# Performance work log

Hardware: AMD Instinct MI355X
Metric: run time of the kernel (lower is better)

## Reference

```python
import jax, jax.numpy as jnp
import numpy as np

N = 100000   # nodes
E = 1600000  # edges
I_DIM = 512
H_DIM = 64   # hardcoded in GCNEncoder
Z_DIM = 64


def gcn_conv(x, W, b, src, dst, n):
    """GCNConv: D^{-1/2}(A+I)D^{-1/2} X W + b, edge weights = 1."""
    xw = x @ W  # [n, out]
    ones = jnp.ones(src.shape[0], dtype=xw.dtype)
    deg = jax.ops.segment_sum(ones, dst, num_segments=n) + 1.0  # +1 for self-loop
    dinv = jax.lax.rsqrt(deg)
    norm = dinv[src] * dinv[dst]  # [E]
    agg = jax.ops.segment_sum(xw[src] * norm[:, None], dst, num_segments=n)
    agg = agg + xw * (dinv * dinv)[:, None]  # self-loop term, norm = 1/deg
    return agg + b


def setup_inputs() -> dict:
    key = jax.random.key(0)
    ks = jax.random.split(key, 9)
    x = jax.random.normal(ks[0], (N, I_DIM), dtype=jnp.float32)
    edge_index = jax.random.randint(ks[1], (2, E), 0, N, dtype=jnp.int64)
    # glorot-ish init for weights
    W1 = jax.random.normal(ks[2], (I_DIM, H_DIM), jnp.float32) * (1.0 / np.sqrt(I_DIM))
    b1 = jnp.zeros((H_DIM,), jnp.float32)
    W_mu = jax.random.normal(ks[3], (H_DIM, Z_DIM), jnp.float32) * (1.0 / np.sqrt(H_DIM))
    b_mu = jnp.zeros((Z_DIM,), jnp.float32)
    W_var = jax.random.normal(ks[4], (H_DIM, Z_DIM), jnp.float32) * (1.0 / np.sqrt(H_DIM))
    b_var = jnp.zeros((Z_DIM,), jnp.float32)
    eps = jax.random.normal(ks[5], (N, Z_DIM), jnp.float32)  # reparameterization noise
    return {"x": x, "edge_index": edge_index, "W1": W1, "b1": b1,
            "W_mu": W_mu, "b_mu": b_mu, "W_var": W_var, "b_var": b_var,
            "eps": eps}


def reference(x, edge_index, W1, b1, W_mu, b_mu, W_var, b_var, eps):
    n = x.shape[0]
    src, dst = edge_index[0], edge_index[1]
    # encoder (eval mode: dropout is identity)
    h = jax.nn.relu(gcn_conv(x, W1, b1, src, dst, n))
    z_mean = gcn_conv(h, W_mu, b_mu, src, dst, n)
    z_var = jax.nn.softplus(gcn_conv(h, W_var, b_var, src, dst, n))
    # Normal(z_mean, z_var).rsample()
    z = z_mean + z_var * eps
    return z_mean, z_var, z
```

## Files before the change

### kernel.cpp

```cpp
#include <hip/hip_runtime.h>
#include <hip/hip_bf16.h>
#include <math.h>

#define IDIM 512
#define HDIM 64

#define CB_SH 9
#define CB_NODES 512
#define PCHUNK 4096

typedef __attribute__((ext_vector_type(8))) short short8;
typedef __attribute__((ext_vector_type(4))) float f32x4;
typedef unsigned short u16;
typedef unsigned int u32;

__device__ __forceinline__ float bflo(u32 u) { return __uint_as_float(u << 16); }
__device__ __forceinline__ float bfhi(u32 u) { return __uint_as_float(u & 0xffff0000u); }


__global__ __launch_bounds__(256) void k_chist(const int* __restrict__ dst,
                                               int* __restrict__ gHist, int E, int NB) {
    __shared__ int h[1024];
    int tid = threadIdx.x;
    for (int i = tid; i < NB; i += 256) h[i] = 0;
    __syncthreads();
    int stride = gridDim.x * 256;
    for (int e = blockIdx.x * 256 + tid; e < E; e += stride)
        atomicAdd(&h[dst[e] >> CB_SH], 1);
    __syncthreads();
    for (int i = tid; i < NB; i += 256)
        if (h[i]) atomicAdd(&gHist[i], h[i]);
}

__global__ __launch_bounds__(256) void k_cscan(const int* __restrict__ gHist,
                                               int* __restrict__ bucketBase,
                                               int* __restrict__ gcur, int NB,
                                               int* __restrict__ rowptr, int n, int E) {
    __shared__ int ss[256];
    int tid = threadIdx.x;
    int v[4];
    int s = 0;
#pragma unroll
    for (int k = 0; k < 4; k++) {
        int i = tid * 4 + k;
        v[k] = (i < NB) ? gHist[i] : 0;
        s += v[k];
    }
    ss[tid] = s;
    __syncthreads();
    for (int o = 1; o < 256; o <<= 1) {
        int u = (tid >= o) ? ss[tid - o] : 0;
        __syncthreads();
        ss[tid] += u;
        __syncthreads();
    }
    int ex = ss[tid] - s;
#pragma unroll
    for (int k = 0; k < 4; k++) {
        int i = tid * 4 + k;
        if (i < NB) { bucketBase[i] = ex; gcur[i] = ex; }
        ex += v[k];
    }
    if (tid == 0) { bucketBase[NB] = E; rowptr[n] = E; }
}

__global__ __launch_bounds__(256) void k_partition(const int* __restrict__ src,
                                                   const int* __restrict__ dst,
                                                   int* __restrict__ gcur,
                                                   int2* __restrict__ tmp, int E, int NB) {
    __shared__ int h[1024];
    __shared__ int base[1024];
    int tid = threadIdx.x;
    int e0 = blockIdx.x * PCHUNK;
    int e1 = min(e0 + PCHUNK, E);
    for (int i = tid; i < NB; i += 256) h[i] = 0;
    __syncthreads();
    for (int e = e0 + tid; e < e1; e += 256)
        atomicAdd(&h[dst[e] >> CB_SH], 1);
    __syncthreads();
    for (int i = tid; i < NB; i += 256) {
        int c = h[i];
        base[i] = c ? atomicAdd(&gcur[i], c) : 0;
        h[i] = 0;
    }
    __syncthreads();
    for (int e = e0 + tid; e < e1; e += 256) {
        int d = dst[e];
        int b = d >> CB_SH;
        int r = atomicAdd(&h[b], 1);
        tmp[base[b] + r] = make_int2(src[e], d);
    }
}

__global__ __launch_bounds__(256) void k_finalize(const int2* __restrict__ tmp,
                                                  const int* __restrict__ bucketBase,
                                                  int* __restrict__ rowptr,
                                                  float* __restrict__ dinv,
                                                  int* __restrict__ srcs, int n) {
    __shared__ int hist[CB_NODES];
    __shared__ int off[CB_NODES];
    __shared__ int ss[256];
    int b = blockIdx.x;
    int tid = threadIdx.x;
    int node0 = b << CB_SH;
    int nloc = min(CB_NODES, n - node0);
    int e0 = bucketBase[b], e1 = bucketBase[b + 1];
    hist[tid] = 0;
    hist[tid + 256] = 0;
    __syncthreads();
    for (int e = e0 + tid; e < e1; e += 256)
        atomicAdd(&hist[tmp[e].y - node0], 1);
    __syncthreads();
    int v0 = hist[2 * tid], v1 = hist[2 * tid + 1];
    int ps = v0 + v1;
    ss[tid] = ps;
    __syncthreads();
    for (int o = 1; o < 256; o <<= 1) {
        int u = (tid >= o) ? ss[tid - o] : 0;
        __syncthreads();
        ss[tid] += u;
        __syncthreads();
    }
    int ex = ss[tid] - ps;
    off[2 * tid] = ex;
    off[2 * tid + 1] = ex + v0;
    __syncthreads();
    for (int i = tid; i < nloc; i += 256) {
        rowptr[node0 + i] = e0 + off[i];
        dinv[node0 + i] = rsqrtf((float)hist[i] + 1.0f);
    }
    __syncthreads();
    for (int e = e0 + tid; e < e1; e += 256) {
        int2 p = tmp[e];
        int r = atomicAdd(&off[p.y - node0], 1);
        srcs[e0 + r] = p.x;
    }
}

__global__ __launch_bounds__(256) void k_prepB(const float* __restrict__ W1,
                                               short* __restrict__ Btg) {
    int id = blockIdx.x * 256 + threadIdx.x;
    if (id >= IDIM * HDIM) return;
    int k = id >> 6, nn = id & 63;
    __hip_bfloat16 b = __float2bfloat16(W1[id]);
    Btg[nn * IDIM + k] = *(short*)&b;
}

__global__ __launch_bounds__(256) void k_prepW2(const float* __restrict__ Wmu,
                                                const float* __restrict__ Wvar,
                                                short* __restrict__ Whi,
                                                short* __restrict__ Wlo) {
    int id = blockIdx.x * 256 + threadIdx.x;
    if (id >= 128 * 64) return;
    int c = id >> 6;
    int k = id & 63;
    float wv = (c < 64) ? Wmu[k * 64 + c] : Wvar[k * 64 + (c - 64)];
    __hip_bfloat16 h = __float2bfloat16(wv);
    float hf = __bfloat162float(h);
    __hip_bfloat16 l = __float2bfloat16(wv - hf);
    Whi[c * 64 + k] = *(short*)&h;
    Wlo[c * 64 + k] = *(short*)&l;
}

#define GM 128
#define KC 64
#define APAD 8
__global__ __launch_bounds__(256) void k_gemm1(const float* __restrict__ x,
                                               const short* __restrict__ Btg,
                                               const float* __restrict__ dinv,
                                               u16* __restrict__ g1, int n) {
    __shared__ short As[GM][KC + APAD];
    __shared__ short Bs[HDIM][KC + APAD];
    int tid = threadIdx.x;
    int row0 = blockIdx.x * GM;
    int w = tid >> 6, lane = tid & 63;
    int m = lane & 15, kb = lane >> 4;

    f32x4 acc[2][4];
#pragma unroll
    for (int rb = 0; rb < 2; rb++)
#pragma unroll
        for (int nt = 0; nt < 4; nt++) acc[rb][nt] = (f32x4){0.f, 0.f, 0.f, 0.f};

    for (int kc = 0; kc < IDIM; kc += KC) {
        __syncthreads();
#pragma unroll
        for (int i = 0; i < 8; i++) {
            int idx = tid + i * 256;
            int r = idx >> 4;
            int c4 = idx & 15;
            int grow = row0 + r;
            float4 v = make_float4(0.f, 0.f, 0.f, 0.f);
            if (grow < n) v = *(const float4*)&x[(size_t)grow * IDIM + kc + c4 * 4];
            __hip_bfloat162 h0 = __float22bfloat162_rn(make_float2(v.x, v.y));
            __hip_bfloat162 h1 = __float22bfloat162_rn(make_float2(v.z, v.w));
            int2 p;
            p.x = *(int*)&h0;
            p.y = *(int*)&h1;
            *(int2*)&As[r][c4 * 4] = p;
        }
#pragma unroll
        for (int i = 0; i < 2; i++) {
            int idx = tid + i * 256;
            int r = idx >> 3;
            int u8 = idx & 7;
            float4 v = *(const float4*)&Btg[(size_t)r * IDIM + kc + u8 * 8];
            *(float4*)&Bs[r][u8 * 8] = v;
        }
        __syncthreads();
#pragma unroll
        for (int ks = 0; ks < KC; ks += 32) {
            short8 a0 = *(const short8*)&As[w * 32 + m][ks + kb * 8];
            short8 a1 = *(const short8*)&As[w * 32 + 16 + m][ks + kb * 8];
            short8 b0 = *(const short8*)&Bs[m][ks + kb * 8];
            short8 b1 = *(const short8*)&Bs[16 + m][ks + kb * 8];
            short8 b2 = *(const short8*)&Bs[32 + m][ks + kb * 8];
            short8 b3 = *(const short8*)&Bs[48 + m][ks + kb * 8];
            acc[0][0] = __builtin_amdgcn_mfma_f32_16x16x32_bf16(a0, b0, acc[0][0], 0, 0, 0);
            acc[0][1] = __builtin_amdgcn_mfma_f32_16x16x32_bf16(a0, b1, acc[0][1], 0, 0, 0);
            acc[0][2] = __builtin_amdgcn_mfma_f32_16x16x32_bf16(a0, b2, acc[0][2], 0, 0, 0);
            acc[0][3] = __builtin_amdgcn_mfma_f32_16x16x32_bf16(a0, b3, acc[0][3], 0, 0, 0);
            acc[1][0] = __builtin_amdgcn_mfma_f32_16x16x32_bf16(a1, b0, acc[1][0], 0, 0, 0);
            acc[1][1] = __builtin_amdgcn_mfma_f32_16x16x32_bf16(a1, b1, acc[1][1], 0, 0, 0);
            acc[1][2] = __builtin_amdgcn_mfma_f32_16x16x32_bf16(a1, b2, acc[1][2], 0, 0, 0);
            acc[1][3] = __builtin_amdgcn_mfma_f32_16x16x32_bf16(a1, b3, acc[1][3], 0, 0, 0);
        }
    }
#pragma unroll
    for (int rb = 0; rb < 2; rb++) {
        int rbase = row0 + w * 32 + rb * 16 + kb * 4;
#pragma unroll
        for (int reg = 0; reg < 4; reg++) {
            int grow = rbase + reg;
            if (grow < n) {
                float dv = dinv[grow];
#pragma unroll
                for (int nt = 0; nt < 4; nt++) {
                    __hip_bfloat16 b = __float2bfloat16(acc[rb][nt][reg] * dv);
                    g1[(size_t)grow * HDIM + nt * 16 + m] = *(u16*)&b;
                }
            }
        }
    }
}

__global__ __launch_bounds__(256) void k_gather1(const int* __restrict__ rowptr,
                                                 const int* __restrict__ srcs,
                                                 const float* __restrict__ dinv,
                                                 const u16* __restrict__ g1,
                                                 const float* __restrict__ b1,
                                                 u16* __restrict__ g2, int n) {
    int tid = threadIdx.x;
    int r = tid >> 6, lane = tid & 63;
    int grp = lane >> 3, q = lane & 7;
    int i = blockIdx.x * 4 + r;
    if (i >= n) return;
    int beg = rowptr[i], end = rowptr[i + 1];
    float a[8];
#pragma unroll
    for (int k = 0; k < 8; k++) a[k] = 0.f;
    int j = beg + grp;
    for (; j + 8 < end; j += 16) {
        int s0 = srcs[j];
        int s1 = srcs[j + 8];
        uint4 u0 = *(const uint4*)&g1[(size_t)s0 * HDIM + q * 8];
        uint4 u1 = *(const uint4*)&g1[(size_t)s1 * HDIM + q * 8];
        a[0] += bflo(u0.x) + bflo(u1.x); a[1] += bfhi(u0.x) + bfhi(u1.x);
        a[2] += bflo(u0.y) + bflo(u1.y); a[3] += bfhi(u0.y) + bfhi(u1.y);
        a[4] += bflo(u0.z) + bflo(u1.z); a[5] += bfhi(u0.z) + bfhi(u1.z);
        a[6] += bflo(u0.w) + bflo(u1.w); a[7] += bfhi(u0.w) + bfhi(u1.w);
    }
    if (j < end) {
        int s0 = srcs[j];
        uint4 u0 = *(const uint4*)&g1[(size_t)s0 * HDIM + q * 8];
        a[0] += bflo(u0.x); a[1] += bfhi(u0.x);
        a[2] += bflo(u0.y); a[3] += bfhi(u0.y);
        a[4] += bflo(u0.z); a[5] += bfhi(u0.z);
        a[6] += bflo(u0.w); a[7] += bfhi(u0.w);
    }
#pragma unroll
    for (int k = 0; k < 8; k++) {
        a[k] += __shfl_xor(a[k], 8);
        a[k] += __shfl_xor(a[k], 16);
        a[k] += __shfl_xor(a[k], 32);
    }
    if (grp == 0) {
        uint4 us = *(const uint4*)&g1[(size_t)i * HDIM + q * 8];
        float s0 = bflo(us.x), s1 = bfhi(us.x), s2 = bflo(us.y), s3 = bfhi(us.y);
        float s4 = bflo(us.z), s5 = bfhi(us.z), s6 = bflo(us.w), s7 = bfhi(us.w);
        float4 bv0 = *(const float4*)&b1[q * 8];
        float4 bv1 = *(const float4*)&b1[q * 8 + 4];
        float di = dinv[i];
        float o0 = fmaxf(di * (a[0] + s0) + bv0.x, 0.f) * di;
        float o1 = fmaxf(di * (a[1] + s1) + bv0.y, 0.f) * di;
        float o2 = fmaxf(di * (a[2] + s2) + bv0.z, 0.f) * di;
        float o3 = fmaxf(di * (a[3] + s3) + bv0.w, 0.f) * di;
        float o4 = fmaxf(di * (a[4] + s4) + bv1.x, 0.f) * di;
        float o5 = fmaxf(di * (a[5] + s5) + bv1.y, 0.f) * di;
        float o6 = fmaxf(di * (a[6] + s6) + bv1.z, 0.f) * di;
        float o7 = fmaxf(di * (a[7] + s7) + bv1.w, 0.f) * di;
        __hip_bfloat162 p0 = __float22bfloat162_rn(make_float2(o0, o1));
        __hip_bfloat162 p1 = __float22bfloat162_rn(make_float2(o2, o3));
        __hip_bfloat162 p2 = __float22bfloat162_rn(make_float2(o4, o5));
        __hip_bfloat162 p3 = __float22bfloat162_rn(make_float2(o6, o7));
        uint4 w;
        w.x = *(u32*)&p0; w.y = *(u32*)&p1; w.z = *(u32*)&p2; w.w = *(u32*)&p3;
        *(uint4*)&g2[(size_t)i * HDIM + q * 8] = w;
    }
}

__global__ __launch_bounds__(256) void k_gather2(const int* __restrict__ rowptr,
                                                 const int* __restrict__ srcs,
                                                 const float* __restrict__ dinv,
                                                 const u16* __restrict__ g2,
                                                 float* __restrict__ hagg, int n) {
    int tid = threadIdx.x;
    int r = tid >> 6, lane = tid & 63;
    int grp = lane >> 3, q = lane & 7;
    int i = blockIdx.x * 4 + r;
    if (i >= n) return;
    int beg = rowptr[i], end = rowptr[i + 1];
    float a[8];
#pragma unroll
    for (int k = 0; k < 8; k++) a[k] = 0.f;
    int j = beg + grp;
    for (; j + 8 < end; j += 16) {
        int s0 = srcs[j];
        int s1 = srcs[j + 8];
        uint4 u0 = *(const uint4*)&g2[(size_t)s0 * HDIM + q * 8];
        uint4 u1 = *(const uint4*)&g2[(size_t)s1 * HDIM + q * 8];
        a[0] += bflo(u0.x) + bflo(u1.x); a[1] += bfhi(u0.x) + bfhi(u1.x);
        a[2] += bflo(u0.y) + bflo(u1.y); a[3] += bfhi(u0.y) + bfhi(u1.y);
        a[4] += bflo(u0.z) + bflo(u1.z); a[5] += bfhi(u0.z) + bfhi(u1.z);
        a[6] += bflo(u0.w) + bflo(u1.w); a[7] += bfhi(u0.w) + bfhi(u1.w);
    }
    if (j < end) {
        int s0 = srcs[j];
        uint4 u0 = *(const uint4*)&g2[(size_t)s0 * HDIM + q * 8];
        a[0] += bflo(u0.x); a[1] += bfhi(u0.x);
        a[2] += bflo(u0.y); a[3] += bfhi(u0.y);
        a[4] += bflo(u0.z); a[5] += bfhi(u0.z);
        a[6] += bflo(u0.w); a[7] += bfhi(u0.w);
    }
#pragma unroll
    for (int k = 0; k < 8; k++) {
        a[k] += __shfl_xor(a[k], 8);
        a[k] += __shfl_xor(a[k], 16);
        a[k] += __shfl_xor(a[k], 32);
    }
    if (grp == 0) {
        uint4 us = *(const uint4*)&g2[(size_t)i * HDIM + q * 8];
        float di = dinv[i];
        float4 o0, o1;
        o0.x = di * (a[0] + bflo(us.x));
        o0.y = di * (a[1] + bfhi(us.x));
        o0.z = di * (a[2] + bflo(us.y));
        o0.w = di * (a[3] + bfhi(us.y));
        o1.x = di * (a[4] + bflo(us.z));
        o1.y = di * (a[5] + bfhi(us.z));
        o1.z = di * (a[6] + bflo(us.w));
        o1.w = di * (a[7] + bfhi(us.w));
        *(float4*)&hagg[(size_t)i * HDIM + q * 8] = o0;
        *(float4*)&hagg[(size_t)i * HDIM + q * 8 + 4] = o1;
    }
}

__global__ __launch_bounds__(256) void k_gemm2(const float* __restrict__ hagg,
                                               const short* __restrict__ Whi,
                                               const short* __restrict__ Wlo,
                                               const float* __restrict__ bmu,
                                               const float* __restrict__ bvar,
                                               const float* __restrict__ eps,
                                               float* __restrict__ out, int n) {
    int tid = threadIdx.x;
    int w = tid >> 6, lane = tid & 63;
    int m = lane & 15, kb = lane >> 4;
    int row0 = blockIdx.x * 128 + w * 32;

    short8 ah[2][2], al[2][2];
#pragma unroll
    for (int rb = 0; rb < 2; rb++) {
#pragma unroll
        for (int ks = 0; ks < 2; ks++) {
            int grow = row0 + rb * 16 + m;
            float v[8];
            if (grow < n) {
                const float* base = &hagg[(size_t)grow * HDIM + ks * 32 + kb * 8];
                float4 v0 = *(const float4*)base;
                float4 v1 = *(const float4*)(base + 4);
                v[0] = v0.x; v[1] = v0.y; v[2] = v0.z; v[3] = v0.w;
                v[4] = v1.x; v[5] = v1.y; v[6] = v1.z; v[7] = v1.w;
            } else {
#pragma unroll
                for (int jj = 0; jj < 8; jj++) v[jj] = 0.f;
            }
#pragma unroll
            for (int jj = 0; jj < 8; jj++) {
                __hip_bfloat16 h = __float2bfloat16(v[jj]);
                float hf = __bfloat162float(h);
                __hip_bfloat16 l = __float2bfloat16(v[jj] - hf);
                ah[rb][ks][jj] = *(short*)&h;
                al[rb][ks][jj] = *(short*)&l;
            }
        }
    }

    f32x4 acc[2][8];
#pragma unroll
    for (int rb = 0; rb < 2; rb++)
#pragma unroll
        for (int nt = 0; nt < 8; nt++) acc[rb][nt] = (f32x4){0.f, 0.f, 0.f, 0.f};

#pragma unroll
    for (int nt = 0; nt < 8; nt++) {
#pragma unroll
        for (int ks = 0; ks < 2; ks++) {
            const short* bbase = &Whi[(size_t)(nt * 16 + m) * HDIM + ks * 32 + kb * 8];
            const short* lbase = &Wlo[(size_t)(nt * 16 + m) * HDIM + ks * 32 + kb * 8];
            short8 bh = *(const short8*)bbase;
            short8 bl = *(const short8*)lbase;
#pragma unroll
            for (int rb = 0; rb < 2; rb++) {
                acc[rb][nt] = __builtin_amdgcn_mfma_f32_16x16x32_bf16(ah[rb][ks], bh, acc[rb][nt], 0, 0, 0);
                acc[rb][nt] = __builtin_amdgcn_mfma_f32_16x16x32_bf16(al[rb][ks], bh, acc[rb][nt], 0, 0, 0);
                acc[rb][nt] = __builtin_amdgcn_mfma_f32_16x16x32_bf16(ah[rb][ks], bl, acc[rb][nt], 0, 0, 0);
            }
        }
    }

    size_t nh = (size_t)n * HDIM;
#pragma unroll
    for (int rb = 0; rb < 2; rb++) {
#pragma unroll
        for (int nt = 0; nt < 4; nt++) {
            int c = nt * 16 + m;
            float bm = bmu[c], bv = bvar[c];
#pragma unroll
            for (int reg = 0; reg < 4; reg++) {
                int grow = row0 + rb * 16 + kb * 4 + reg;
                if (grow < n) {
                    float mu = acc[rb][nt][reg] + bm;
                    float va = acc[rb][nt + 4][reg] + bv;
                    float zv = fmaxf(va, 0.f) + log1pf(expf(-fabsf(va)));
                    size_t o = (size_t)grow * HDIM + c;
                    float z = mu + zv * eps[o];
                    out[o] = mu;
                    out[nh + o] = zv;
                    out[2 * nh + o] = z;
                }
            }
        }
    }
}

extern "C" void kernel_launch(void* const* d_in, const int* in_sizes, int n_in,
                              void* d_out, int out_size, void* d_ws, size_t ws_size,
                              hipStream_t stream) {
    const float* x    = (const float*)d_in[0];
    const int*   ei   = (const int*)d_in[1];
    const float* W1   = (const float*)d_in[2];
    const float* b1   = (const float*)d_in[3];
    const float* Wmu  = (const float*)d_in[4];
    const float* bmu  = (const float*)d_in[5];
    const float* Wvar = (const float*)d_in[6];
    const float* bvar = (const float*)d_in[7];
    const float* eps  = (const float*)d_in[8];
    float* out = (float*)d_out;

    int n = in_sizes[0] / IDIM;
    int E = in_sizes[1] / 2;
    const int* src = ei;
    const int* dst = ei + E;

    int NB = (n + CB_NODES - 1) >> CB_SH;

    char* p = (char*)d_ws;
    u16* bufB   = (u16*)p;               p += (size_t)n * HDIM * 2;
    float* hagg = (float*)p;             p += (size_t)n * HDIM * 4;
    u16* bufA   = (u16*)hagg;
    int2* tmp   = (int2*)hagg;
    int* srcs   = (int*)p;               p += (size_t)E * 4;
    short* Btg  = (short*)p;             p += (size_t)IDIM * HDIM * 2;
    short* W2hi = (short*)p;             p += (size_t)128 * HDIM * 2;
    short* W2lo = (short*)p;             p += (size_t)128 * HDIM * 2;
    int* rowptr = (int*)p;               p += (size_t)(n + 1) * 4;
    float* dinv = (float*)p;             p += (size_t)n * 4;
    int* gHist  = (int*)p;               p += 1024 * 4;
    int* gcur   = (int*)p;               p += 1024 * 4;
    int* bucketBase = (int*)p;           p += 1025 * 4;

    hipMemsetAsync(gHist, 0, (size_t)NB * sizeof(int), stream);
    k_chist<<<512, 256, 0, stream>>>(dst, gHist, E, NB);
    k_cscan<<<1, 256, 0, stream>>>(gHist, bucketBase, gcur, NB, rowptr, n, E);
    k_partition<<<(E + PCHUNK - 1) / PCHUNK, 256, 0, stream>>>(src, dst, gcur, tmp, E, NB);
    k_finalize<<<NB, 256, 0, stream>>>(tmp, bucketBase, rowptr, dinv, srcs, n);

    k_prepB<<<(IDIM * HDIM + 255) / 256, 256, 0, stream>>>(W1, Btg);
    k_prepW2<<<(128 * HDIM + 255) / 256, 256, 0, stream>>>(Wmu, Wvar, W2hi, W2lo);

    k_gemm1<<<(n + GM - 1) / GM, 256, 0, stream>>>(x, Btg, dinv, bufA, n);
    k_gather1<<<(n + 3) / 4, 256, 0, stream>>>(rowptr, srcs, dinv, bufA, b1, bufB, n);

    k_gather2<<<(n + 3) / 4, 256, 0, stream>>>(rowptr, srcs, dinv, bufB, hagg, n);
    k_gemm2<<<(n + 127) / 128, 256, 0, stream>>>(hagg, W2hi, W2lo, bmu, bvar, eps, out, n);
}
```

Baseline: 574.0 us.

## Split gather feature tables into 16-column slabs processed in separate grid passes

The first GEMM now writes its bf16 output as four column-major slabs of 16 features per node instead of 64-feature rows. Both gather kernels launch a 2D grid with one y-slice per slab, so each pass reads a 32-byte slab per neighbour. The goal is a smaller per-pass working set (about 3.2MB instead of 12.8MB) that fits better in L2 for random neighbour access. In exchange, rowptr and srcs are read four times, loads shrink to 4 bytes per lane, and many more blocks are launched.

```diff
diff --git a/kernel.cpp b/kernel.cpp
--- a/kernel.cpp
+++ b/kernel.cpp
@@ -237,7 +237,7 @@
 #pragma unroll
                 for (int nt = 0; nt < 4; nt++) {
                     __hip_bfloat16 b = __float2bfloat16(acc[rb][nt][reg] * dv);
-                    g1[(size_t)grow * HDIM + nt * 16 + m] = *(u16*)&b;
+                    g1[((size_t)nt * n + grow) * 16 + m] = *(u16*)&b;
                 }
             }
         }
@@ -247,121 +247,83 @@
 __global__ __launch_bounds__(256) void k_gather1(const int* __restrict__ rowptr,
                                                  const int* __restrict__ srcs,
                                                  const float* __restrict__ dinv,
-                                                 const u16* __restrict__ g1,
+                                                 const u16* __restrict__ g1s,
                                                  const float* __restrict__ b1,
-                                                 u16* __restrict__ g2, int n) {
+                                                 u16* __restrict__ g2s, int n) {
+    int pass = blockIdx.y;
+    const u16* T = g1s + (size_t)pass * n * 16;
+    u16* O = g2s + (size_t)pass * n * 16;
     int tid = threadIdx.x;
     int r = tid >> 6, lane = tid & 63;
     int grp = lane >> 3, q = lane & 7;
     int i = blockIdx.x * 4 + r;
     if (i >= n) return;
     int beg = rowptr[i], end = rowptr[i + 1];
-    float a[8];
-#pragma unroll
-    for (int k = 0; k < 8; k++) a[k] = 0.f;
+    float a0 = 0.f, a1 = 0.f;
     int j = beg + grp;
     for (; j + 8 < end; j += 16) {
         int s0 = srcs[j];
         int s1 = srcs[j + 8];
-        uint4 u0 = *(const uint4*)&g1[(size_t)s0 * HDIM + q * 8];
-        uint4 u1 = *(const uint4*)&g1[(size_t)s1 * HDIM + q * 8];
-        a[0] += bflo(u0.x) + bflo(u1.x); a[1] += bfhi(u0.x) + bfhi(u1.x);
-        a[2] += bflo(u0.y) + bflo(u1.y); a[3] += bfhi(u0.y) + bfhi(u1.y);
-        a[4] += bflo(u0.z) + bflo(u1.z); a[5] += bfhi(u0.z) + bfhi(u1.z);
-        a[6] += bflo(u0.w) + bflo(u1.w); a[7] += bfhi(u0.w) + bfhi(u1.w);
+        u32 u0 = *(const u32*)&T[(size_t)s0 * 16 + q * 2];
+        u32 u1 = *(const u32*)&T[(size_t)s1 * 16 + q * 2];
+        a0 += bflo(u0) + bflo(u1);
+        a1 += bfhi(u0) + bfhi(u1);
     }
     if (j < end) {
-        int s0 = srcs[j];
-        uint4 u0 = *(const uint4*)&g1[(size_t)s0 * HDIM + q * 8];
-        a[0] += bflo(u0.x); a[1] += bfhi(u0.x);
-        a[2] += bflo(u0.y); a[3] += bfhi(u0.y);
-        a[4] += bflo(u0.z); a[5] += bfhi(u0.z);
-        a[6] += bflo(u0.w); a[7] += bfhi(u0.w);
-    }
-#pragma unroll
-    for (int k = 0; k < 8; k++) {
-        a[k] += __shfl_xor(a[k], 8);
-        a[k] += __shfl_xor(a[k], 16);
-        a[k] += __shfl_xor(a[k], 32);
-    }
+        u32 u0 = *(const u32*)&T[(size_t)srcs[j] * 16 + q * 2];
+        a0 += bflo(u0);
+        a1 += bfhi(u0);
+    }
+    a0 += __shfl_xor(a0, 8); a0 += __shfl_xor(a0, 16); a0 += __shfl_xor(a0, 32);
+    a1 += __shfl_xor(a1, 8); a1 += __shfl_xor(a1, 16); a1 += __shfl_xor(a1, 32);
     if (grp == 0) {
-        uint4 us = *(const uint4*)&g1[(size_t)i * HDIM + q * 8];
-        float s0 = bflo(us.x), s1 = bfhi(us.x), s2 = bflo(us.y), s3 = bfhi(us.y);
-        float s4 = bflo(us.z), s5 = bfhi(us.z), s6 = bflo(us.w), s7 = bfhi(us.w);
-        float4 bv0 = *(const float4*)&b1[q * 8];
-        float4 bv1 = *(const float4*)&b1[q * 8 + 4];
+        u32 us = *(const u32*)&T[(size_t)i * 16 + q * 2];
+        float2 bv = *(const float2*)&b1[pass * 16 + q * 2];
         float di = dinv[i];
-        float o0 = fmaxf(di * (a[0] + s0) + bv0.x, 0.f) * di;
-        float o1 = fmaxf(di * (a[1] + s1) + bv0.y, 0.f) * di;
-        float o2 = fmaxf(di * (a[2] + s2) + bv0.z, 0.f) * di;
-        float o3 = fmaxf(di * (a[3] + s3) + bv0.w, 0.f) * di;
-        float o4 = fmaxf(di * (a[4] + s4) + bv1.x, 0.f) * di;
-        float o5 = fmaxf(di * (a[5] + s5) + bv1.y, 0.f) * di;
-        float o6 = fmaxf(di * (a[6] + s6) + bv1.z, 0.f) * di;
-        float o7 = fmaxf(di * (a[7] + s7) + bv1.w, 0.f) * di;
-        __hip_bfloat162 p0 = __float22bfloat162_rn(make_float2(o0, o1));
-        __hip_bfloat162 p1 = __float22bfloat162_rn(make_float2(o2, o3));
-        __hip_bfloat162 p2 = __float22bfloat162_rn(make_float2(o4, o5));
-        __hip_bfloat162 p3 = __float22bfloat162_rn(make_float2(o6, o7));
-        uint4 w;
-        w.x = *(u32*)&p0; w.y = *(u32*)&p1; w.z = *(u32*)&p2; w.w = *(u32*)&p3;
-        *(uint4*)&g2[(size_t)i * HDIM + q * 8] = w;
+        float o0 = fmaxf(di * (a0 + bflo(us)) + bv.x, 0.f) * di;
+        float o1 = fmaxf(di * (a1 + bfhi(us)) + bv.y, 0.f) * di;
+        __hip_bfloat162 pk = __float22bfloat162_rn(make_float2(o0, o1));
+        *(u32*)&O[(size_t)i * 16 + q * 2] = *(u32*)&pk;
     }
 }
 
 __global__ __launch_bounds__(256) void k_gather2(const int* __restrict__ rowptr,
                                                  const int* __restrict__ srcs,
                                                  const float* __restrict__ dinv,
-                                                 const u16* __restrict__ g2,
+                                                 const u16* __restrict__ g2s,
                                                  float* __restrict__ hagg, int n) {
+    int pass = blockIdx.y;
+    const u16* T = g2s + (size_t)pass * n * 16;
     int tid = threadIdx.x;
     int r = tid >> 6, lane = tid & 63;
     int grp = lane >> 3, q = lane & 7;
     int i = blockIdx.x * 4 + r;
     if (i >= n) return;
     int beg = rowptr[i], end = rowptr[i + 1];
-    float a[8];
-#pragma unroll
-    for (int k = 0; k < 8; k++) a[k] = 0.f;
+    float a0 = 0.f, a1 = 0.f;
     int j = beg + grp;
     for (; j + 8 < end; j += 16) {
         int s0 = srcs[j];
         int s1 = srcs[j + 8];
-        uint4 u0 = *(const uint4*)&g2[(size_t)s0 * HDIM + q * 8];
-        uint4 u1 = *(const uint4*)&g2[(size_t)s1 * HDIM + q * 8];
-        a[0] += bflo(u0.x) + bflo(u1.x); a[1] += bfhi(u0.x) + bfhi(u1.x);
-        a[2] += bflo(u0.y) + bflo(u1.y); a[3] += bfhi(u0.y) + bfhi(u1.y);
-        a[4] += bflo(u0.z) + bflo(u1.z); a[5] += bfhi(u0.z) + bfhi(u1.z);
-        a[6] += bflo(u0.w) + bflo(u1.w); a[7] += bfhi(u0.w) + bfhi(u1.w);
+        u32 u0 = *(const u32*)&T[(size_t)s0 * 16 + q * 2];
+        u32 u1 = *(const u32*)&T[(size_t)s1 * 16 + q * 2];
+        a0 += bflo(u0) + bflo(u1);
+        a1 += bfhi(u0) + bfhi(u1);
     }
     if (j < end) {
-        int s0 = srcs[j];
-        uint4 u0 = *(const uint4*)&g2[(size_t)s0 * HDIM + q * 8];
-        a[0] += bflo(u0.x); a[1] += bfhi(u0.x);
-        a[2] += bflo(u0.y); a[3] += bfhi(u0.y);
-        a[4] += bflo(u0.z); a[5] += bfhi(u0.z);
-        a[6] += bflo(u0.w); a[7] += bfhi(u0.w);
-    }
-#pragma unroll
-    for (int k = 0; k < 8; k++) {
-        a[k] += __shfl_xor(a[k], 8);
-        a[k] += __shfl_xor(a[k], 16);
-        a[k] += __shfl_xor(a[k], 32);
-    }
+        u32 u0 = *(const u32*)&T[(size_t)srcs[j] * 16 + q * 2];
+        a0 += bflo(u0);
+        a1 += bfhi(u0);
+    }
+    a0 += __shfl_xor(a0, 8); a0 += __shfl_xor(a0, 16); a0 += __shfl_xor(a0, 32);
+    a1 += __shfl_xor(a1, 8); a1 += __shfl_xor(a1, 16); a1 += __shfl_xor(a1, 32);
     if (grp == 0) {
-        uint4 us = *(const uint4*)&g2[(size_t)i * HDIM + q * 8];
+        u32 us = *(const u32*)&T[(size_t)i * 16 + q * 2];
         float di = dinv[i];
-        float4 o0, o1;
-        o0.x = di * (a[0] + bflo(us.x));
-        o0.y = di * (a[1] + bfhi(us.x));
-        o0.z = di * (a[2] + bflo(us.y));
-        o0.w = di * (a[3] + bfhi(us.y));
-        o1.x = di * (a[4] + bflo(us.z));
-        o1.y = di * (a[5] + bfhi(us.z));
-        o1.z = di * (a[6] + bflo(us.w));
-        o1.w = di * (a[7] + bfhi(us.w));
-        *(float4*)&hagg[(size_t)i * HDIM + q * 8] = o0;
-        *(float4*)&hagg[(size_t)i * HDIM + q * 8 + 4] = o1;
+        float2 o;
+        o.x = di * (a0 + bflo(us));
+        o.y = di * (a1 + bfhi(us));
+        *(float2*)&hagg[(size_t)i * HDIM + pass * 16 + q * 2] = o;
     }
 }
 
@@ -499,8 +461,9 @@
     k_prepW2<<<(128 * HDIM + 255) / 256, 256, 0, stream>>>(Wmu, Wvar, W2hi, W2lo);
 
     k_gemm1<<<(n + GM - 1) / GM, 256, 0, stream>>>(x, Btg, dinv, bufA, n);
-    k_gather1<<<(n + 3) / 4, 256, 0, stream>>>(rowptr, srcs, dinv, bufA, b1, bufB, n);
-
-    k_gather2<<<(n + 3) / 4, 256, 0, stream>>>(rowptr, srcs, dinv, bufB, hagg, n);
+    dim3 gg((n + 3) / 4, 4);
+    k_gather1<<<gg, 256, 0, stream>>>(rowptr, srcs, dinv, bufA, b1, bufB, n);
+
+    k_gather2<<<gg, 256, 0, stream>>>(rowptr, srcs, dinv, bufB, hagg, n);
     k_gemm2<<<(n + 127) / 128, 256, 0, stream>>>(hagg, W2hi, W2lo, bmu, bvar, eps, out, n);
 }
```

After: 721.2 us. 25.6% more time.

## Split gathers into source-range passes for cache locality with partial accumulation

Applied to the files above, without the earlier changes.

Edges are bucketed by source quarter as well as destination block, giving four CSR row-pointer sets. Each gather then runs as four passes, and each pass reads only a quarter of the feature table so that slice can stay in L2/MALL. Partial sums go through an fp32 scratch buffer using nontemporal loads and stores, and srcs reads are made nontemporal. The cost is more kernel launches, extra read-modify-write traffic on the accumulator, and a separate dinv kernel.

```diff
diff --git a/kernel.cpp b/kernel.cpp
--- a/kernel.cpp
+++ b/kernel.cpp
@@ -6,36 +6,42 @@
 #define HDIM 64
 
 #define CB_SH 9
-#define CB_NODES 512
+#define NSB 4
 #define PCHUNK 4096
 
 typedef __attribute__((ext_vector_type(8))) short short8;
 typedef __attribute__((ext_vector_type(4))) float f32x4;
+typedef __attribute__((ext_vector_type(4))) float f4;
 typedef unsigned short u16;
 typedef unsigned int u32;
 
 __device__ __forceinline__ float bflo(u32 u) { return __uint_as_float(u << 16); }
 __device__ __forceinline__ float bfhi(u32 u) { return __uint_as_float(u & 0xffff0000u); }
-
-
-__global__ __launch_bounds__(256) void k_chist(const int* __restrict__ dst,
-                                               int* __restrict__ gHist, int E, int NB) {
+__device__ __forceinline__ f4 ntload4(const float* p) { return __builtin_nontemporal_load((const f4*)p); }
+__device__ __forceinline__ void ntstore4(float* p, f4 v) { __builtin_nontemporal_store(v, (f4*)p); }
+
+__global__ __launch_bounds__(256) void k_chist(const int* __restrict__ src,
+                                               const int* __restrict__ dst,
+                                               int* __restrict__ gHist, int E,
+                                               int NBK, int NBd, int Q) {
     __shared__ int h[1024];
     int tid = threadIdx.x;
-    for (int i = tid; i < NB; i += 256) h[i] = 0;
+    for (int i = tid; i < NBK; i += 256) h[i] = 0;
     __syncthreads();
     int stride = gridDim.x * 256;
-    for (int e = blockIdx.x * 256 + tid; e < E; e += stride)
-        atomicAdd(&h[dst[e] >> CB_SH], 1);
-    __syncthreads();
-    for (int i = tid; i < NB; i += 256)
+    for (int e = blockIdx.x * 256 + tid; e < E; e += stride) {
+        int key = (src[e] / Q) * NBd + (dst[e] >> CB_SH);
+        atomicAdd(&h[key], 1);
+    }
+    __syncthreads();
+    for (int i = tid; i < NBK; i += 256)
         if (h[i]) atomicAdd(&gHist[i], h[i]);
 }
 
 __global__ __launch_bounds__(256) void k_cscan(const int* __restrict__ gHist,
                                                int* __restrict__ bucketBase,
-                                               int* __restrict__ gcur, int NB,
-                                               int* __restrict__ rowptr, int n, int E) {
+                                               int* __restrict__ gcur, int NBK, int NBd,
+                                               int* __restrict__ rowptr4, int n, int E) {
     __shared__ int ss[256];
     int tid = threadIdx.x;
     int v[4];
@@ -43,7 +49,7 @@
 #pragma unroll
     for (int k = 0; k < 4; k++) {
         int i = tid * 4 + k;
-        v[k] = (i < NB) ? gHist[i] : 0;
+        v[k] = (i < NBK) ? gHist[i] : 0;
         s += v[k];
     }
     ss[tid] = s;
@@ -58,53 +64,64 @@
 #pragma unroll
     for (int k = 0; k < 4; k++) {
         int i = tid * 4 + k;
-        if (i < NB) { bucketBase[i] = ex; gcur[i] = ex; }
+        if (i < NBK) {
+            bucketBase[i] = ex;
+            gcur[i] = ex;
+            if (i > 0 && (i % NBd) == 0)
+                rowptr4[(size_t)(i / NBd - 1) * (n + 1) + n] = ex;
+        }
         ex += v[k];
     }
-    if (tid == 0) { bucketBase[NB] = E; rowptr[n] = E; }
+    if (tid == 0) {
+        bucketBase[NBK] = E;
+        rowptr4[(size_t)(NSB - 1) * (n + 1) + n] = E;
+    }
 }
 
 __global__ __launch_bounds__(256) void k_partition(const int* __restrict__ src,
                                                    const int* __restrict__ dst,
                                                    int* __restrict__ gcur,
-                                                   int2* __restrict__ tmp, int E, int NB) {
+                                                   int2* __restrict__ tmp, int E,
+                                                   int NBK, int NBd, int Q) {
     __shared__ int h[1024];
     __shared__ int base[1024];
     int tid = threadIdx.x;
     int e0 = blockIdx.x * PCHUNK;
     int e1 = min(e0 + PCHUNK, E);
-    for (int i = tid; i < NB; i += 256) h[i] = 0;
-    __syncthreads();
-    for (int e = e0 + tid; e < e1; e += 256)
-        atomicAdd(&h[dst[e] >> CB_SH], 1);
-    __syncthreads();
-    for (int i = tid; i < NB; i += 256) {
+    for (int i = tid; i < NBK; i += 256) h[i] = 0;
+    __syncthreads();
+    for (int e = e0 + tid; e < e1; e += 256) {
+        int key = (src[e] / Q) * NBd + (dst[e] >> CB_SH);
+        atomicAdd(&h[key], 1);
+    }
+    __syncthreads();
+    for (int i = tid; i < NBK; i += 256) {
         int c = h[i];
         base[i] = c ? atomicAdd(&gcur[i], c) : 0;
         h[i] = 0;
     }
     __syncthreads();
     for (int e = e0 + tid; e < e1; e += 256) {
-        int d = dst[e];
-        int b = d >> CB_SH;
-        int r = atomicAdd(&h[b], 1);
-        tmp[base[b] + r] = make_int2(src[e], d);
+        int sv = src[e], d = dst[e];
+        int key = (sv / Q) * NBd + (d >> CB_SH);
+        int r = atomicAdd(&h[key], 1);
+        tmp[base[key] + r] = make_int2(sv, d);
     }
 }
 
 __global__ __launch_bounds__(256) void k_finalize(const int2* __restrict__ tmp,
                                                   const int* __restrict__ bucketBase,
-                                                  int* __restrict__ rowptr,
-                                                  float* __restrict__ dinv,
-                                                  int* __restrict__ srcs, int n) {
-    __shared__ int hist[CB_NODES];
-    __shared__ int off[CB_NODES];
+                                                  int* __restrict__ rowptr4,
+                                                  int* __restrict__ srcs, int n, int NBd) {
+    __shared__ int hist[1 << CB_SH];
+    __shared__ int off[1 << CB_SH];
     __shared__ int ss[256];
-    int b = blockIdx.x;
-    int tid = threadIdx.x;
-    int node0 = b << CB_SH;
-    int nloc = min(CB_NODES, n - node0);
-    int e0 = bucketBase[b], e1 = bucketBase[b + 1];
+    int key = blockIdx.x;
+    int sb = key / NBd, db = key % NBd;
+    int tid = threadIdx.x;
+    int node0 = db << CB_SH;
+    int nloc = min(1 << CB_SH, n - node0);
+    int e0 = bucketBase[key], e1 = bucketBase[key + 1];
     hist[tid] = 0;
     hist[tid + 256] = 0;
     __syncthreads();
@@ -125,16 +142,28 @@
     off[2 * tid] = ex;
     off[2 * tid + 1] = ex + v0;
     __syncthreads();
-    for (int i = tid; i < nloc; i += 256) {
-        rowptr[node0 + i] = e0 + off[i];
-        dinv[node0 + i] = rsqrtf((float)hist[i] + 1.0f);
-    }
+    int* rp = rowptr4 + (size_t)sb * (n + 1);
+    for (int i = tid; i < nloc; i += 256)
+        rp[node0 + i] = e0 + off[i];
     __syncthreads();
     for (int e = e0 + tid; e < e1; e += 256) {
         int2 p = tmp[e];
         int r = atomicAdd(&off[p.y - node0], 1);
         srcs[e0 + r] = p.x;
     }
+}
+
+__global__ __launch_bounds__(256) void k_dinv(const int* __restrict__ rowptr4,
+                                              float* __restrict__ dinv, int n) {
+    int i = blockIdx.x * 256 + threadIdx.x;
+    if (i >= n) return;
+    int d = 0;
+#pragma unroll
+    for (int sb = 0; sb < NSB; sb++) {
+        const int* rp = rowptr4 + (size_t)sb * (n + 1);
+        d += rp[i + 1] - rp[i];
+    }
+    dinv[i] = rsqrtf((float)d + 1.0f);
 }
 
 __global__ __launch_bounds__(256) void k_prepB(const float* __restrict__ W1,
@@ -244,25 +273,28 @@
     }
 }
 
-__global__ __launch_bounds__(256) void k_gather1(const int* __restrict__ rowptr,
-                                                 const int* __restrict__ srcs,
-                                                 const float* __restrict__ dinv,
-                                                 const u16* __restrict__ g1,
-                                                 const float* __restrict__ b1,
-                                                 u16* __restrict__ g2, int n) {
+__global__ __launch_bounds__(256) void k_g1pass(const int* __restrict__ rowptr4,
+                                                const int* __restrict__ srcs,
+                                                const float* __restrict__ dinv,
+                                                const u16* __restrict__ g1,
+                                                const float* __restrict__ b1,
+                                                float* __restrict__ acc1,
+                                                u16* __restrict__ g2, int n,
+                                                int pass, int isFirst, int isLast) {
+    const int* rp = rowptr4 + (size_t)pass * (n + 1);
     int tid = threadIdx.x;
     int r = tid >> 6, lane = tid & 63;
     int grp = lane >> 3, q = lane & 7;
     int i = blockIdx.x * 4 + r;
     if (i >= n) return;
-    int beg = rowptr[i], end = rowptr[i + 1];
+    int beg = rp[i], end = rp[i + 1];
     float a[8];
 #pragma unroll
     for (int k = 0; k < 8; k++) a[k] = 0.f;
     int j = beg + grp;
     for (; j + 8 < end; j += 16) {
-        int s0 = srcs[j];
-        int s1 = srcs[j + 8];
+        int s0 = __builtin_nontemporal_load(&srcs[j]);
+        int s1 = __builtin_nontemporal_load(&srcs[j + 8]);
         uint4 u0 = *(const uint4*)&g1[(size_t)s0 * HDIM + q * 8];
         uint4 u1 = *(const uint4*)&g1[(size_t)s1 * HDIM + q * 8];
         a[0] += bflo(u0.x) + bflo(u1.x); a[1] += bfhi(u0.x) + bfhi(u1.x);
@@ -271,7 +303,7 @@
         a[6] += bflo(u0.w) + bflo(u1.w); a[7] += bfhi(u0.w) + bfhi(u1.w);
     }
     if (j < end) {
-        int s0 = srcs[j];
+        int s0 = __builtin_nontemporal_load(&srcs[j]);
         uint4 u0 = *(const uint4*)&g1[(size_t)s0 * HDIM + q * 8];
         a[0] += bflo(u0.x); a[1] += bfhi(u0.x);
         a[2] += bflo(u0.y); a[3] += bfhi(u0.y);
@@ -285,48 +317,64 @@
         a[k] += __shfl_xor(a[k], 32);
     }
     if (grp == 0) {
-        uint4 us = *(const uint4*)&g1[(size_t)i * HDIM + q * 8];
-        float s0 = bflo(us.x), s1 = bfhi(us.x), s2 = bflo(us.y), s3 = bfhi(us.y);
-        float s4 = bflo(us.z), s5 = bfhi(us.z), s6 = bflo(us.w), s7 = bfhi(us.w);
-        float4 bv0 = *(const float4*)&b1[q * 8];
-        float4 bv1 = *(const float4*)&b1[q * 8 + 4];
-        float di = dinv[i];
-        float o0 = fmaxf(di * (a[0] + s0) + bv0.x, 0.f) * di;
-        float o1 = fmaxf(di * (a[1] + s1) + bv0.y, 0.f) * di;
-        float o2 = fmaxf(di * (a[2] + s2) + bv0.z, 0.f) * di;
-        float o3 = fmaxf(di * (a[3] + s3) + bv0.w, 0.f) * di;
-        float o4 = fmaxf(di * (a[4] + s4) + bv1.x, 0.f) * di;
-        float o5 = fmaxf(di * (a[5] + s5) + bv1.y, 0.f) * di;
-        float o6 = fmaxf(di * (a[6] + s6) + bv1.z, 0.f) * di;
-        float o7 = fmaxf(di * (a[7] + s7) + bv1.w, 0.f) * di;
-        __hip_bfloat162 p0 = __float22bfloat162_rn(make_float2(o0, o1));
-        __hip_bfloat162 p1 = __float22bfloat162_rn(make_float2(o2, o3));
-        __hip_bfloat162 p2 = __float22bfloat162_rn(make_float2(o4, o5));
-        __hip_bfloat162 p3 = __float22bfloat162_rn(make_float2(o6, o7));
-        uint4 w;
-        w.x = *(u32*)&p0; w.y = *(u32*)&p1; w.z = *(u32*)&p2; w.w = *(u32*)&p3;
-        *(uint4*)&g2[(size_t)i * HDIM + q * 8] = w;
-    }
-}
-
-__global__ __launch_bounds__(256) void k_gather2(const int* __restrict__ rowptr,
-                                                 const int* __restrict__ srcs,
-                                                 const float* __restrict__ dinv,
-                                                 const u16* __restrict__ g2,
-                                                 float* __restrict__ hagg, int n) {
+        size_t base = (size_t)i * HDIM + q * 8;
+        if (!isFirst) {
+            f4 p0 = ntload4(&acc1[base]);
+            f4 p1 = ntload4(&acc1[base + 4]);
+            a[0] += p0[0]; a[1] += p0[1]; a[2] += p0[2]; a[3] += p0[3];
+            a[4] += p1[0]; a[5] += p1[1]; a[6] += p1[2]; a[7] += p1[3];
+        }
+        if (!isLast) {
+            f4 s0v = {a[0], a[1], a[2], a[3]};
+            f4 s1v = {a[4], a[5], a[6], a[7]};
+            ntstore4(&acc1[base], s0v);
+            ntstore4(&acc1[base + 4], s1v);
+        } else {
+            uint4 us = *(const uint4*)&g1[base];
+            float s0 = bflo(us.x), s1 = bfhi(us.x), s2 = bflo(us.y), s3 = bfhi(us.y);
+            float s4 = bflo(us.z), s5 = bfhi(us.z), s6 = bflo(us.w), s7 = bfhi(us.w);
+            float4 bv0 = *(const float4*)&b1[q * 8];
+            float4 bv1 = *(const float4*)&b1[q * 8 + 4];
+            float di = dinv[i];
+            float o0 = fmaxf(di * (a[0] + s0) + bv0.x, 0.f) * di;
+            float o1 = fmaxf(di * (a[1] + s1) + bv0.y, 0.f) * di;
+            float o2 = fmaxf(di * (a[2] + s2) + bv0.z, 0.f) * di;
+            float o3 = fmaxf(di * (a[3] + s3) + bv0.w, 0.f) * di;
+            float o4 = fmaxf(di * (a[4] + s4) + bv1.x, 0.f) * di;
+            float o5 = fmaxf(di * (a[5] + s5) + bv1.y, 0.f) * di;
+            float o6 = fmaxf(di * (a[6] + s6) + bv1.z, 0.f) * di;
+            float o7 = fmaxf(di * (a[7] + s7) + bv1.w, 0.f) * di;
+            __hip_bfloat162 p0 = __float22bfloat162_rn(make_float2(o0, o1));
+            __hip_bfloat162 p1 = __float22bfloat162_rn(make_float2(o2, o3));
+            __hip_bfloat162 p2 = __float22bfloat162_rn(make_float2(o4, o5));
+            __hip_bfloat162 p3 = __float22bfloat162_rn(make_float2(o6, o7));
+            uint4 w;
+            w.x = *(u32*)&p0; w.y = *(u32*)&p1; w.z = *(u32*)&p2; w.w = *(u32*)&p3;
+            *(uint4*)&g2[base] = w;
+        }
+    }
+}
+
+__global__ __launch_bounds__(256) void k_g2pass(const int* __restrict__ rowptr4,
+                                                const int* __restrict__ srcs,
+                                                const float* __restrict__ dinv,
+                                                const u16* __restrict__ g2,
+                                                float* __restrict__ hagg, int n,
+                                                int pass, int isFirst, int isLast) {
+    const int* rp = rowptr4 + (size_t)pass * (n + 1);
     int tid = threadIdx.x;
     int r = tid >> 6, lane = tid & 63;
     int grp = lane >> 3, q = lane & 7;
     int i = blockIdx.x * 4 + r;
     if (i >= n) return;
-    int beg = rowptr[i], end = rowptr[i + 1];
+    int beg = rp[i], end = rp[i + 1];
     float a[8];
 #pragma unroll
     for (int k = 0; k < 8; k++) a[k] = 0.f;
     int j = beg + grp;
     for (; j + 8 < end; j += 16) {
-        int s0 = srcs[j];
-        int s1 = srcs[j + 8];
+        int s0 = __builtin_nontemporal_load(&srcs[j]);
+        int s1 = __builtin_nontemporal_load(&srcs[j + 8]);
         uint4 u0 = *(const uint4*)&g2[(size_t)s0 * HDIM + q * 8];
         uint4 u1 = *(const uint4*)&g2[(size_t)s1 * HDIM + q * 8];
         a[0] += bflo(u0.x) + bflo(u1.x); a[1] += bfhi(u0.x) + bfhi(u1.x);
@@ -335,7 +383,7 @@
         a[6] += bflo(u0.w) + bflo(u1.w); a[7] += bfhi(u0.w) + bfhi(u1.w);
     }
     if (j < end) {
-        int s0 = srcs[j];
+        int s0 = __builtin_nontemporal_load(&srcs[j]);
         uint4 u0 = *(const uint4*)&g2[(size_t)s0 * HDIM + q * 8];
         a[0] += bflo(u0.x); a[1] += bfhi(u0.x);
         a[2] += bflo(u0.y); a[3] += bfhi(u0.y);
@@ -349,19 +397,33 @@
         a[k] += __shfl_xor(a[k], 32);
     }
     if (grp == 0) {
-        uint4 us = *(const uint4*)&g2[(size_t)i * HDIM + q * 8];
-        float di = dinv[i];
-        float4 o0, o1;
-        o0.x = di * (a[0] + bflo(us.x));
-        o0.y = di * (a[1] + bfhi(us.x));
-        o0.z = di * (a[2] + bflo(us.y));
-        o0.w = di * (a[3] + bfhi(us.y));
-        o1.x = di * (a[4] + bflo(us.z));
-        o1.y = di * (a[5] + bfhi(us.z));
-        o1.z = di * (a[6] + bflo(us.w));
-        o1.w = di * (a[7] + bfhi(us.w));
-        *(float4*)&hagg[(size_t)i * HDIM + q * 8] = o0;
-        *(float4*)&hagg[(size_t)i * HDIM + q * 8 + 4] = o1;
+        size_t base = (size_t)i * HDIM + q * 8;
+        if (!isFirst) {
+            f4 p0 = ntload4(&hagg[base]);
+            f4 p1 = ntload4(&hagg[base + 4]);
+            a[0] += p0[0]; a[1] += p0[1]; a[2] += p0[2]; a[3] += p0[3];
+            a[4] += p1[0]; a[5] += p1[1]; a[6] += p1[2]; a[7] += p1[3];
+        }
+        if (!isLast) {
+            f4 s0v = {a[0], a[1], a[2], a[3]};
+            f4 s1v = {a[4], a[5], a[6], a[7]};
+            ntstore4(&hagg[base], s0v);
+            ntstore4(&hagg[base + 4], s1v);
+        } else {
+            uint4 us = *(const uint4*)&g2[base];
+            float di = dinv[i];
+            f4 o0, o1;
+            o0[0] = di * (a[0] + bflo(us.x));
+            o0[1] = di * (a[1] + bfhi(us.x));
+            o0[2] = di * (a[2] + bflo(us.y));
+            o0[3] = di * (a[3] + bfhi(us.y));
+            o1[0] = di * (a[4] + bflo(us.z));
+            o1[1] = di * (a[5] + bfhi(us.z));
+            o1[2] = di * (a[6] + bflo(us.w));
+            o1[3] = di * (a[7] + bfhi(us.w));
+            ntstore4(&hagg[base], o0);
+            ntstore4(&hagg[base + 4], o1);
+        }
     }
 }
 
@@ -472,35 +534,44 @@
     const int* src = ei;
     const int* dst = ei + E;
 
-    int NB = (n + CB_NODES - 1) >> CB_SH;
+    int NBd = (n + (1 << CB_SH) - 1) >> CB_SH;
+    int NBK = NSB * NBd;
+    int Q   = (n + NSB - 1) / NSB;
 
     char* p = (char*)d_ws;
     u16* bufB   = (u16*)p;               p += (size_t)n * HDIM * 2;
     float* hagg = (float*)p;             p += (size_t)n * HDIM * 4;
     u16* bufA   = (u16*)hagg;
     int2* tmp   = (int2*)hagg;
+    float* acc1 = (float*)p;             p += (size_t)n * HDIM * 4;
     int* srcs   = (int*)p;               p += (size_t)E * 4;
     short* Btg  = (short*)p;             p += (size_t)IDIM * HDIM * 2;
     short* W2hi = (short*)p;             p += (size_t)128 * HDIM * 2;
     short* W2lo = (short*)p;             p += (size_t)128 * HDIM * 2;
-    int* rowptr = (int*)p;               p += (size_t)(n + 1) * 4;
+    int* rowptr4 = (int*)p;              p += (size_t)NSB * (n + 1) * 4;
     float* dinv = (float*)p;             p += (size_t)n * 4;
     int* gHist  = (int*)p;               p += 1024 * 4;
     int* gcur   = (int*)p;               p += 1024 * 4;
     int* bucketBase = (int*)p;           p += 1025 * 4;
 
-    hipMemsetAsync(gHist, 0, (size_t)NB * sizeof(int), stream);
-    k_chist<<<512, 256, 0, stream>>>(dst, gHist, E, NB);
-    k_cscan<<<1, 256, 0, stream>>>(gHist, bucketBase, gcur, NB, rowptr, n, E);
-    k_partition<<<(E + PCHUNK - 1) / PCHUNK, 256, 0, stream>>>(src, dst, gcur, tmp, E, NB);
-    k_finalize<<<NB, 256, 0, stream>>>(tmp, bucketBase, rowptr, dinv, srcs, n);
+    hipMemsetAsync(gHist, 0, (size_t)NBK * sizeof(int), stream);
+    k_chist<<<512, 256, 0, stream>>>(src, dst, gHist, E, NBK, NBd, Q);
+    k_cscan<<<1, 256, 0, stream>>>(gHist, bucketBase, gcur, NBK, NBd, rowptr4, n, E);
+    k_partition<<<(E + PCHUNK - 1) / PCHUNK, 256, 0, stream>>>(src, dst, gcur, tmp, E, NBK, NBd, Q);
+    k_finalize<<<NBK, 256, 0, stream>>>(tmp, bucketBase, rowptr4, srcs, n, NBd);
+    k_dinv<<<(n + 255) / 256, 256, 0, stream>>>(rowptr4, dinv, n);
 
     k_prepB<<<(IDIM * HDIM + 255) / 256, 256, 0, stream>>>(W1, Btg);
     k_prepW2<<<(128 * HDIM + 255) / 256, 256, 0, stream>>>(Wmu, Wvar, W2hi, W2lo);
 
     k_gemm1<<<(n + GM - 1) / GM, 256, 0, stream>>>(x, Btg, dinv, bufA, n);
-    k_gather1<<<(n + 3) / 4, 256, 0, stream>>>(rowptr, srcs, dinv, bufA, b1, bufB, n);
-
-    k_gather2<<<(n + 3) / 4, 256, 0, stream>>>(rowptr, srcs, dinv, bufB, hagg, n);
+    int gga = (n + 3) / 4;
+    for (int sb = 0; sb < NSB; sb++)
+        k_g1pass<<<gga, 256, 0, stream>>>(rowptr4, srcs, dinv, bufA, b1, acc1, bufB,
+                                          n, sb, sb == 0, sb == NSB - 1);
+
+    for (int sb = 0; sb < NSB; sb++)
+        k_g2pass<<<gga, 256, 0, stream>>>(rowptr4, srcs, dinv, bufB, hagg,
+                                          n, sb, sb == 0, sb == NSB - 1);
     k_gemm2<<<(n + 127) / 128, 256, 0, stream>>>(hagg, W2hi, W2lo, bmu, bvar, eps, out, n);
 }
```

New measurement: 788.2 us. +37.3%, slower.

## Prefetch gemm1 tiles into registers and pack edge temp into 32-bit words

Applied to the files above, without the earlier changes.

The first GEMM now loads the next K-chunk of x and W1 into registers while the current chunk is computed from shared memory. This overlaps global loads with MFMA work at the cost of more registers. The edge partition buffer now stores src and the local dst offset packed in one 32-bit word instead of an int2, halving that traffic. The bucket scan kernel is also shrunk to 128 threads, which caps it at 256 buckets.

```diff
diff --git a/kernel.cpp b/kernel.cpp
--- a/kernel.cpp
+++ b/kernel.cpp
@@ -32,23 +32,23 @@
         if (h[i]) atomicAdd(&gHist[i], h[i]);
 }
 
-__global__ __launch_bounds__(256) void k_cscan(const int* __restrict__ gHist,
+__global__ __launch_bounds__(128) void k_cscan(const int* __restrict__ gHist,
                                                int* __restrict__ bucketBase,
                                                int* __restrict__ gcur, int NB,
                                                int* __restrict__ rowptr, int n, int E) {
-    __shared__ int ss[256];
-    int tid = threadIdx.x;
-    int v[4];
+    __shared__ int ss[128];
+    int tid = threadIdx.x;
+    int v[2];
     int s = 0;
 #pragma unroll
-    for (int k = 0; k < 4; k++) {
-        int i = tid * 4 + k;
+    for (int k = 0; k < 2; k++) {
+        int i = tid * 2 + k;
         v[k] = (i < NB) ? gHist[i] : 0;
         s += v[k];
     }
     ss[tid] = s;
     __syncthreads();
-    for (int o = 1; o < 256; o <<= 1) {
+    for (int o = 1; o < 128; o <<= 1) {
         int u = (tid >= o) ? ss[tid - o] : 0;
         __syncthreads();
         ss[tid] += u;
@@ -56,8 +56,8 @@
     }
     int ex = ss[tid] - s;
 #pragma unroll
-    for (int k = 0; k < 4; k++) {
-        int i = tid * 4 + k;
+    for (int k = 0; k < 2; k++) {
+        int i = tid * 2 + k;
         if (i < NB) { bucketBase[i] = ex; gcur[i] = ex; }
         ex += v[k];
     }
@@ -67,7 +67,7 @@
 __global__ __launch_bounds__(256) void k_partition(const int* __restrict__ src,
                                                    const int* __restrict__ dst,
                                                    int* __restrict__ gcur,
-                                                   int2* __restrict__ tmp, int E, int NB) {
+                                                   u32* __restrict__ tmp, int E, int NB) {
     __shared__ int h[1024];
     __shared__ int base[1024];
     int tid = threadIdx.x;
@@ -88,11 +88,11 @@
         int d = dst[e];
         int b = d >> CB_SH;
         int r = atomicAdd(&h[b], 1);
-        tmp[base[b] + r] = make_int2(src[e], d);
-    }
-}
-
-__global__ __launch_bounds__(256) void k_finalize(const int2* __restrict__ tmp,
+        tmp[base[b] + r] = ((u32)src[e] << CB_SH) | (u32)(d & (CB_NODES - 1));
+    }
+}
+
+__global__ __launch_bounds__(256) void k_finalize(const u32* __restrict__ tmp,
                                                   const int* __restrict__ bucketBase,
                                                   int* __restrict__ rowptr,
                                                   float* __restrict__ dinv,
@@ -109,7 +109,7 @@
     hist[tid + 256] = 0;
     __syncthreads();
     for (int e = e0 + tid; e < e1; e += 256)
-        atomicAdd(&hist[tmp[e].y - node0], 1);
+        atomicAdd(&hist[tmp[e] & (CB_NODES - 1)], 1);
     __syncthreads();
     int v0 = hist[2 * tid], v1 = hist[2 * tid + 1];
     int ps = v0 + v1;
@@ -131,9 +131,9 @@
     }
     __syncthreads();
     for (int e = e0 + tid; e < e1; e += 256) {
-        int2 p = tmp[e];
-        int r = atomicAdd(&off[p.y - node0], 1);
-        srcs[e0 + r] = p.x;
+        u32 p = tmp[e];
+        int r = atomicAdd(&off[p & (CB_NODES - 1)], 1);
+        srcs[e0 + r] = (int)(p >> CB_SH);
     }
 }
 
@@ -176,38 +176,56 @@
     int w = tid >> 6, lane = tid & 63;
     int m = lane & 15, kb = lane >> 4;
 
+    int ar = tid >> 4;
+    int ac4 = tid & 15;
+    int br = tid >> 3;
+    int bu8 = tid & 7;
+
     f32x4 acc[2][4];
 #pragma unroll
     for (int rb = 0; rb < 2; rb++)
 #pragma unroll
         for (int nt = 0; nt < 4; nt++) acc[rb][nt] = (f32x4){0.f, 0.f, 0.f, 0.f};
 
+    float4 pa[8];
+    float4 pb[2];
+#pragma unroll
+    for (int i = 0; i < 8; i++) {
+        int grow = row0 + ar + i * 16;
+        pa[i] = (grow < n) ? *(const float4*)&x[(size_t)grow * IDIM + ac4 * 4]
+                           : make_float4(0.f, 0.f, 0.f, 0.f);
+    }
+#pragma unroll
+    for (int i = 0; i < 2; i++)
+        pb[i] = *(const float4*)&Btg[(size_t)(br + i * 32) * IDIM + bu8 * 8];
+
     for (int kc = 0; kc < IDIM; kc += KC) {
+#pragma unroll
+        for (int i = 0; i < 8; i++) {
+            __hip_bfloat162 h0 = __float22bfloat162_rn(make_float2(pa[i].x, pa[i].y));
+            __hip_bfloat162 h1 = __float22bfloat162_rn(make_float2(pa[i].z, pa[i].w));
+            int2 pp;
+            pp.x = *(int*)&h0;
+            pp.y = *(int*)&h1;
+            *(int2*)&As[ar + i * 16][ac4 * 4] = pp;
+        }
+#pragma unroll
+        for (int i = 0; i < 2; i++)
+            *(float4*)&Bs[br + i * 32][bu8 * 8] = pb[i];
         __syncthreads();
-#pragma unroll
-        for (int i = 0; i < 8; i++) {
-            int idx = tid + i * 256;
-            int r = idx >> 4;
-            int c4 = idx & 15;
-            int grow = row0 + r;
-            float4 v = make_float4(0.f, 0.f, 0.f, 0.f);
-            if (grow < n) v = *(const float4*)&x[(size_t)grow * IDIM + kc + c4 * 4];
-            __hip_bfloat162 h0 = __float22bfloat162_rn(make_float2(v.x, v.y));
-            __hip_bfloat162 h1 = __float22bfloat162_rn(make_float2(v.z, v.w));
-            int2 p;
-            p.x = *(int*)&h0;
-            p.y = *(int*)&h1;
-            *(int2*)&As[r][c4 * 4] = p;
-        }
-#pragma unroll
-        for (int i = 0; i < 2; i++) {
-            int idx = tid + i * 256;
-            int r = idx >> 3;
-            int u8 = idx & 7;
-            float4 v = *(const float4*)&Btg[(size_t)r * IDIM + kc + u8 * 8];
-            *(float4*)&Bs[r][u8 * 8] = v;
-        }
-        __syncthreads();
+
+        if (kc + KC < IDIM) {
+#pragma unroll
+            for (int i = 0; i < 8; i++) {
+                int grow = row0 + ar + i * 16;
+                pa[i] = (grow < n) ? *(const float4*)&x[(size_t)grow * IDIM + kc + KC + ac4 * 4]
+                                   : make_float4(0.f, 0.f, 0.f, 0.f);
+            }
+#pragma unroll
+            for (int i = 0; i < 2; i++)
+                pb[i] = *(const float4*)&Btg[(size_t)(br + i * 32) * IDIM + kc + KC + bu8 * 8];
+        }
+
 #pragma unroll
         for (int ks = 0; ks < KC; ks += 32) {
             short8 a0 = *(const short8*)&As[w * 32 + m][ks + kb * 8];
@@ -225,6 +243,7 @@
             acc[1][2] = __builtin_amdgcn_mfma_f32_16x16x32_bf16(a1, b2, acc[1][2], 0, 0, 0);
             acc[1][3] = __builtin_amdgcn_mfma_f32_16x16x32_bf16(a1, b3, acc[1][3], 0, 0, 0);
         }
+        __syncthreads();
     }
 #pragma unroll
     for (int rb = 0; rb < 2; rb++) {
@@ -478,7 +497,7 @@
     u16* bufB   = (u16*)p;               p += (size_t)n * HDIM * 2;
     float* hagg = (float*)p;             p += (size_t)n * HDIM * 4;
     u16* bufA   = (u16*)hagg;
-    int2* tmp   = (int2*)hagg;
+    u32* tmp    = (u32*)hagg;
     int* srcs   = (int*)p;               p += (size_t)E * 4;
     short* Btg  = (short*)p;             p += (size_t)IDIM * HDIM * 2;
     short* W2hi = (short*)p;             p += (size_t)128 * HDIM * 2;
@@ -491,7 +510,7 @@
 
     hipMemsetAsync(gHist, 0, (size_t)NB * sizeof(int), stream);
     k_chist<<<512, 256, 0, stream>>>(dst, gHist, E, NB);
-    k_cscan<<<1, 256, 0, stream>>>(gHist, bucketBase, gcur, NB, rowptr, n, E);
+    k_cscan<<<1, 128, 0, stream>>>(gHist, bucketBase, gcur, NB, rowptr, n, E);
     k_partition<<<(E + PCHUNK - 1) / PCHUNK, 256, 0, stream>>>(src, dst, gcur, tmp, E, NB);
     k_finalize<<<NB, 256, 0, stream>>>(tmp, bucketBase, rowptr, dinv, srcs, n);
 
```

After: 614.9 us. +7.1%, slower.
